# Optimization experiments

Measured on AMD Instinct MI355X. Metric: run time of the kernel, lower is better.

The kernel has to match this reference:

```python
import jax, jax.numpy as jnp
import numpy as np

N_NODES = 100000
N_EDGES = 1600000
HIDDEN = 128
N_CLASSES = 40
# torch.rand(1).item() in apply_randalign; fixed here for a deterministic reference
ALPHA = 0.62


def setup_inputs() -> dict:
    key = jax.random.key(0)
    ks = jax.random.split(key, 6)
    inputs = jax.random.normal(ks[0], (N_NODES, HIDDEN), jnp.float32)
    src = jax.random.randint(ks[1], (N_EDGES,), 0, N_NODES, jnp.int32)
    dst = jax.random.randint(ks[2], (N_EDGES,), 0, N_NODES, jnp.int32)
    s = 1.0 / np.sqrt(HIDDEN)
    W1 = jax.random.normal(ks[3], (HIDDEN, HIDDEN), jnp.float32) * s
    W2 = jax.random.normal(ks[4], (HIDDEN, HIDDEN), jnp.float32) * s
    W3 = jax.random.normal(ks[5], (HIDDEN, N_CLASSES), jnp.float32) * s
    return dict(inputs=inputs, src=src, dst=dst,
                W1=W1, b1=jnp.zeros((HIDDEN,), jnp.float32),
                W2=W2, b2=jnp.zeros((HIDDEN,), jnp.float32),
                W3=W3, b3=jnp.zeros((N_CLASSES,), jnp.float32))


def _graph_conv(x, W, b, src, dst):
    # DGL GraphConv, norm='both': D_dst^{-1/2} A D_src^{-1/2} X W + b
    n = x.shape[0]
    ones = jnp.ones(src.shape, x.dtype)
    deg_out = jnp.clip(jax.ops.segment_sum(ones, src, num_segments=n), 1.0)
    deg_in = jnp.clip(jax.ops.segment_sum(ones, dst, num_segments=n), 1.0)
    h = (x @ W) * (deg_out ** -0.5)[:, None]          # row scaling commutes with XW
    agg = jax.ops.segment_sum(h[src], dst, num_segments=n)
    return agg * (deg_in ** -0.5)[:, None] + b


def _randalign(h_prev, h_curr, alpha):
    norm_prev = jnp.linalg.norm(h_prev, axis=1, keepdims=True)
    norm_curr = jnp.linalg.norm(h_curr, axis=1, keepdims=True)
    scaled_prev = h_prev * (norm_curr / norm_prev)
    return alpha * h_curr + (1.0 - alpha) * scaled_prev


def reference(inputs, src, dst, W1, b1, W2, b2, W3, b3):
    # Faithful to source: layers[0] is never applied; loop runs over layers[1..-2].
    h = jax.nn.relu(_graph_conv(inputs, W1, b1, src, dst))      # i = 1
    h_next = jax.nn.relu(_graph_conv(h, W2, b2, src, dst))      # i = 2
    h = _randalign(h, h_next, ALPHA)
    logits = _graph_conv(h, W3, b3, src, dst)                   # final layer
    return logits
```

## Files before the change

kernel.cpp:

```cpp
#include <hip/hip_runtime.h>
#include <hip/hip_bf16.h>

#define HIDDEN 128
#define ALPHA_F 0.62f
#define CAP 64
#define BKT_BITS 9
#define BCAP 10240
#define CSTRIDE 136

typedef __attribute__((ext_vector_type(8))) short bf16x8;
typedef __attribute__((ext_vector_type(4))) float f32x4;

__device__ inline unsigned short f2bf(float f) {
  unsigned u = __float_as_uint(f);
  unsigned r = (u + 0x7fffu + ((u >> 16) & 1u)) >> 16;
  return (unsigned short)r;
}
__device__ inline float bf2f(unsigned short h) {
  return __uint_as_float((unsigned)h << 16);
}
__device__ inline float bflo(unsigned x) { return __uint_as_float(x << 16); }
__device__ inline float bfhi(unsigned x) { return __uint_as_float(x & 0xffff0000u); }

__device__ inline f32x4 mfma_bf16(bf16x8 a, bf16x8 b, f32x4 c) {
  return __builtin_amdgcn_mfma_f32_16x16x32_bf16(a, b, c, 0, 0, 0);
}

template <int CT>
__device__ void gemm_mfma_body(const float* __restrict__ A,
                               const unsigned short* __restrict__ WhT,
                               const unsigned short* __restrict__ WlT,
                               unsigned short* __restrict__ outp, int n, int NW, int gi,
                               unsigned* __restrict__ smem) {
  unsigned short* s16 = (unsigned short*)smem;
  const int t = threadIdx.x;
  const int wv = t >> 6, l = t & 63;
  const int lr = l & 15, lg = (l >> 4) & 3;
  const int rb = gi * 128;

  constexpr int WSLOTS = 4 * CT * 64;
  for (int s = t; s < WSLOTS; s += 256) {
    int sl = s & 63;
    int cc = s >> 6;
    int ct = cc % CT, c = cc / CT;
    int col = ct * 16 + (sl & 15);
    int k = c * 32 + ((sl >> 4) & 3) * 8;
    uint4 hv = *(const uint4*)&WhT[(size_t)col * HIDDEN + k];
    uint4 lv = *(const uint4*)&WlT[(size_t)col * HIDDEN + k];
    *(uint4*)&s16[(cc * 2 + 0) * 512 + sl * 8] = hv;
    *(uint4*)&s16[(cc * 2 + 1) * 512 + sl * 8] = lv;
  }

  f32x4 acc[2][CT];
#pragma unroll
  for (int rt = 0; rt < 2; rt++)
#pragma unroll
    for (int ct = 0; ct < CT; ct++)
#pragma unroll
      for (int e = 0; e < 4; e++) acc[rt][ct][e] = 0.f;

  __syncthreads();

  for (int c = 0; c < 4; c++) {
    bf16x8 ah[2], al[2];
#pragma unroll
    for (int rt = 0; rt < 2; rt++) {
      int rr = rb + wv * 32 + rt * 16 + lr;
      if (rr >= n) rr = n - 1;
      const float4* g = (const float4*)(A + (size_t)rr * HIDDEN + c * 32 + lg * 8);
      float4 v0 = g[0], v1 = g[1];
      float f[8] = {v0.x, v0.y, v0.z, v0.w, v1.x, v1.y, v1.z, v1.w};
#pragma unroll
      for (int q = 0; q < 8; q++) {
        unsigned short h = f2bf(f[q]);
        ah[rt][q] = (short)h;
        al[rt][q] = (short)f2bf(f[q] - bf2f(h));
      }
    }
#pragma unroll
    for (int ct = 0; ct < CT; ct++) {
      int cc = c * CT + ct;
      bf16x8 bh = *(const bf16x8*)&s16[(cc * 2 + 0) * 512 + l * 8];
      bf16x8 bl = *(const bf16x8*)&s16[(cc * 2 + 1) * 512 + l * 8];
#pragma unroll
      for (int rt = 0; rt < 2; rt++) {
        acc[rt][ct] = mfma_bf16(ah[rt], bh, acc[rt][ct]);
        acc[rt][ct] = mfma_bf16(al[rt], bh, acc[rt][ct]);
        acc[rt][ct] = mfma_bf16(ah[rt], bl, acc[rt][ct]);
      }
    }
  }

  __syncthreads();
  unsigned short* cr = s16 + wv * (32 * CSTRIDE);
#pragma unroll
  for (int rt = 0; rt < 2; rt++)
#pragma unroll
    for (int ct = 0; ct < CT; ct++)
#pragma unroll
      for (int r = 0; r < 4; r++)
        cr[(rt * 16 + lg * 4 + r) * CSTRIDE + ct * 16 + lr] = f2bf(acc[rt][ct][r]);
#pragma unroll
  for (int ps = 0; ps < 8; ps++) {
    int row_local = ps * 4 + lg;
    int orow = rb + wv * 32 + row_local;
    if (orow < n && lr * 8 < NW) {
      uint4 v = *(const uint4*)&cr[row_local * CSTRIDE + lr * 8];
      *(uint4*)&outp[(size_t)orow * NW + lr * 8] = v;
    }
  }
}

__global__ __launch_bounds__(256) void partition_kernel(
    const int* __restrict__ src, const int* __restrict__ dst, int E, int nbkt,
    unsigned* __restrict__ gcur1, unsigned* __restrict__ gcur2,
    unsigned* __restrict__ stg1, unsigned short* __restrict__ stg2, int pa_blocks,
    const float* __restrict__ W1, const float* __restrict__ W2, const float* __restrict__ W3,
    unsigned short* __restrict__ W1h, unsigned short* __restrict__ W1l,
    unsigned short* __restrict__ W2h, unsigned short* __restrict__ W2l,
    unsigned short* __restrict__ W3h, unsigned short* __restrict__ W3l, int NC) {
  const int t = threadIdx.x;
  const int bid = blockIdx.x;
  if (bid >= pa_blocks) {
    int r = bid - pa_blocks;
    const float* W = (r == 0) ? W1 : (r == 1) ? W2 : W3;
    unsigned short* Wh = (r == 0) ? W1h : (r == 1) ? W2h : W3h;
    unsigned short* Wl = (r == 0) ? W1l : (r == 1) ? W2l : W3l;
    int ncol = (r == 2) ? 64 : 128;
    int nw   = (r == 2) ? NC : 128;
    for (int idx = t; idx < ncol * HIDDEN; idx += 256) {
      int c = idx >> 7, k = idx & 127;
      float v = (c < nw) ? W[(size_t)k * nw + c] : 0.f;
      unsigned short hi = f2bf(v);
      Wh[idx] = hi;
      Wl[idx] = f2bf(v - bf2f(hi));
    }
    return;
  }
  __shared__ unsigned h1[256], h2[256], b1[256], b2[256];
  h1[t] = 0; h2[t] = 0;
  __syncthreads();
  const int chunk = (E + pa_blocks - 1) / pa_blocks;
  const int e0 = bid * chunk, e1 = min(e0 + chunk, E);
  for (int e = e0 + t; e < e1; e += 256) {
    atomicAdd(&h1[(unsigned)dst[e] >> BKT_BITS], 1u);
    atomicAdd(&h2[(unsigned)src[e] >> BKT_BITS], 1u);
  }
  __syncthreads();
  if (t < nbkt) {
    b1[t] = atomicAdd(&gcur1[t], h1[t]);
    b2[t] = atomicAdd(&gcur2[t], h2[t]);
  }
  h1[t] = 0; h2[t] = 0;
  __syncthreads();
  for (int e = e0 + t; e < e1; e += 256) {
    int s = src[e], d = dst[e];
    unsigned bk1 = (unsigned)d >> BKT_BITS;
    unsigned p1 = b1[bk1] + atomicAdd(&h1[bk1], 1u);
    if (p1 < BCAP) stg1[(size_t)bk1 * BCAP + p1] = ((unsigned)s << BKT_BITS) | ((unsigned)d & 511u);
    unsigned bk2 = (unsigned)s >> BKT_BITS;
    unsigned p2 = b2[bk2] + atomicAdd(&h2[bk2], 1u);
    if (p2 < BCAP) stg2[(size_t)bk2 * BCAP + p2] = (unsigned short)(s & 511);
  }
}

__global__ __launch_bounds__(256) void csr_and_gemm1_kernel(
    const unsigned* __restrict__ gcur1, const unsigned* __restrict__ gcur2,
    const unsigned* __restrict__ stg1, const unsigned short* __restrict__ stg2,
    int* __restrict__ csr, int* __restrict__ deg_in, int* __restrict__ deg_out,
    int n, int nbkt,
    const float* __restrict__ X,
    const unsigned short* __restrict__ W1h, const unsigned short* __restrict__ W1l,
    unsigned short* __restrict__ T1) {
  __shared__ __align__(16) unsigned smem[16384];
  const int bid = blockIdx.x;
  if (bid >= 2 * nbkt) {
    gemm_mfma_body<8>(X, W1h, W1l, T1, n, HIDDEN, bid - 2 * nbkt, smem);
    return;
  }
  int* cnt = (int*)smem;
  const int t = threadIdx.x;
  cnt[t] = 0; cnt[t + 256] = 0;
  __syncthreads();
  if (bid < nbkt) {
    const int b = bid;
    const int m = min((int)gcur1[b], BCAP);
    const int node0 = b << BKT_BITS;
    for (int i = t; i < m; i += 256) {
      unsigned val = stg1[(size_t)b * BCAP + i];
      int dl = val & 511;
      int s = (int)(val >> BKT_BITS);
      int pos = atomicAdd(&cnt[dl], 1);
      if (pos < CAP) csr[((size_t)(node0 + dl) << 6) + pos] = s;
    }
    __syncthreads();
    for (int u = t; u < 512; u += 256) {
      int node = node0 + u;
      if (node < n) deg_in[node] = cnt[u];
    }
  } else {
    const int b = bid - nbkt;
    const int m = min((int)gcur2[b], BCAP);
    const int node0 = b << BKT_BITS;
    for (int i = t; i < m; i += 256) {
      atomicAdd(&cnt[stg2[(size_t)b * BCAP + i]], 1);
    }
    __syncthreads();
    for (int u = t; u < 512; u += 256) {
      int node = node0 + u;
      if (node < n) deg_out[node] = cnt[u];
    }
  }
}

__global__ __launch_bounds__(256) void gemm2_kernel(
    const float* __restrict__ A,
    const unsigned short* __restrict__ Wh, const unsigned short* __restrict__ Wl,
    unsigned short* __restrict__ T, int n) {
  __shared__ __align__(16) unsigned smem[16384];
  gemm_mfma_body<8>(A, Wh, Wl, T, n, HIDDEN, blockIdx.x, smem);
}

__global__ __launch_bounds__(256) void gemm3_kernel(
    const float* __restrict__ A,
    const unsigned short* __restrict__ Wh, const unsigned short* __restrict__ Wl,
    unsigned short* __restrict__ T, int n) {
  __shared__ __align__(16) unsigned smem[9000];
  gemm_mfma_body<4>(A, Wh, Wl, T, n, 64, blockIdx.x, smem);
}

template <bool RA>
__global__ __launch_bounds__(256) void gather_conv_kernel(
    const unsigned* __restrict__ Tu, const int* __restrict__ csr,
    const int* __restrict__ deg_out, const int* __restrict__ deg_in,
    const float* __restrict__ bias, float* __restrict__ H, int n) {
  const int wv = threadIdx.x >> 6, l = threadIdx.x & 63;
  const int v = blockIdx.x * 4 + wv;
  if (v >= n) return;
  const int half = l >> 5, cg = l & 31;
  const int deg = deg_in[v];
  const int m = min(deg, CAP);
  int iu = (l < m) ? csr[((size_t)v << 6) + l] : 0;
  float wu = (l < m) ? rsqrtf((float)max(deg_out[iu], 1)) : 0.f;

  const uint2* Tr = (const uint2*)Tu;
  float a0 = 0.f, a1 = 0.f, a2 = 0.f, a3 = 0.f;
  float b0 = 0.f, b1 = 0.f, b2 = 0.f, b3 = 0.f;
  int j = 0;
  for (; j + 2 < m; j += 4) {
    int eA = j + half, eB = j + 2 + half;
    int uA = __shfl(iu, eA), uB = __shfl(iu, eB);
    float wA = __shfl(wu, eA), wB = __shfl(wu, eB);
    uint2 xA = Tr[(size_t)uA * 32 + cg];
    uint2 xB = Tr[(size_t)uB * 32 + cg];
    a0 = fmaf(wA, bflo(xA.x), a0); a1 = fmaf(wA, bfhi(xA.x), a1);
    a2 = fmaf(wA, bflo(xA.y), a2); a3 = fmaf(wA, bfhi(xA.y), a3);
    b0 = fmaf(wB, bflo(xB.x), b0); b1 = fmaf(wB, bfhi(xB.x), b1);
    b2 = fmaf(wB, bflo(xB.y), b2); b3 = fmaf(wB, bfhi(xB.y), b3);
  }
  for (; j < m; j += 2) {
    int eA = j + half;
    int uA = __shfl(iu, eA);
    float wA = __shfl(wu, eA);
    uint2 xA = Tr[(size_t)uA * 32 + cg];
    a0 = fmaf(wA, bflo(xA.x), a0); a1 = fmaf(wA, bfhi(xA.x), a1);
    a2 = fmaf(wA, bflo(xA.y), a2); a3 = fmaf(wA, bfhi(xA.y), a3);
  }
  a0 += b0; a1 += b1; a2 += b2; a3 += b3;
  a0 += __shfl_xor(a0, 32);
  a1 += __shfl_xor(a1, 32);
  a2 += __shfl_xor(a2, 32);
  a3 += __shfl_xor(a3, 32);

  float din = rsqrtf((float)max(deg, 1));
  float4 bias4 = ((const float4*)bias)[cg];
  float r0 = fmaxf(a0 * din + bias4.x, 0.f);
  float r1 = fmaxf(a1 * din + bias4.y, 0.f);
  float r2 = fmaxf(a2 * din + bias4.z, 0.f);
  float r3 = fmaxf(a3 * din + bias4.w, 0.f);

  if (RA) {
    float4 p = ((const float4*)(H + (size_t)v * HIDDEN))[cg];
    float sc = r0 * r0 + r1 * r1 + r2 * r2 + r3 * r3;
    float sp = p.x * p.x + p.y * p.y + p.z * p.z + p.w * p.w;
#pragma unroll
    for (int off = 1; off < 32; off <<= 1) {
      sc += __shfl_xor(sc, off);
      sp += __shfl_xor(sp, off);
    }
    float ratio = sqrtf(sc) / sqrtf(sp);
    r0 = ALPHA_F * r0 + (1.0f - ALPHA_F) * p.x * ratio;
    r1 = ALPHA_F * r1 + (1.0f - ALPHA_F) * p.y * ratio;
    r2 = ALPHA_F * r2 + (1.0f - ALPHA_F) * p.z * ratio;
    r3 = ALPHA_F * r3 + (1.0f - ALPHA_F) * p.w * ratio;
  }
  if (half == 0)
    ((float4*)(H + (size_t)v * HIDDEN))[cg] = make_float4(r0, r1, r2, r3);
}

__global__ __launch_bounds__(256) void gather_final_kernel(
    const unsigned* __restrict__ Tu3, const int* __restrict__ csr,
    const int* __restrict__ deg_out, const int* __restrict__ deg_in,
    const float* __restrict__ bias, float* __restrict__ out, int n, int NC) {
  const int wv = threadIdx.x >> 6, l = threadIdx.x & 63;
  const int v = blockIdx.x * 4 + wv;
  if (v >= n) return;
  const int q = l >> 4, cg = l & 15;
  const int deg = deg_in[v];
  const int m = min(deg, CAP);
  int iu = (l < m) ? csr[((size_t)v << 6) + l] : 0;
  float wu = (l < m) ? rsqrtf((float)max(deg_out[iu], 1)) : 0.f;

  const uint2* Tr = (const uint2*)Tu3;
  float a0 = 0.f, a1 = 0.f, a2 = 0.f, a3 = 0.f;
  for (int j = 0; j < m; j += 4) {
    int e = j + q;
    int u = __shfl(iu, e);
    float w = __shfl(wu, e);
    uint2 x = Tr[(size_t)u * 16 + cg];
    a0 = fmaf(w, bflo(x.x), a0); a1 = fmaf(w, bfhi(x.x), a1);
    a2 = fmaf(w, bflo(x.y), a2); a3 = fmaf(w, bfhi(x.y), a3);
  }
  a0 += __shfl_xor(a0, 16); a0 += __shfl_xor(a0, 32);
  a1 += __shfl_xor(a1, 16); a1 += __shfl_xor(a1, 32);
  a2 += __shfl_xor(a2, 16); a2 += __shfl_xor(a2, 32);
  a3 += __shfl_xor(a3, 16); a3 += __shfl_xor(a3, 32);
  if (l < 10) {
    float din = rsqrtf((float)max(deg, 1));
    float4 bias4 = ((const float4*)bias)[l];
    float4 o = make_float4(a0 * din + bias4.x, a1 * din + bias4.y,
                           a2 * din + bias4.z, a3 * din + bias4.w);
    *(float4*)(out + (size_t)v * NC + 4 * l) = o;
  }
}

extern "C" void kernel_launch(void* const* d_in, const int* in_sizes, int n_in,
                              void* d_out, int out_size, void* d_ws, size_t ws_size,
                              hipStream_t stream) {
  const float* X  = (const float*)d_in[0];
  const int* src  = (const int*)d_in[1];
  const int* dst  = (const int*)d_in[2];
  const float* W1 = (const float*)d_in[3];
  const float* b1 = (const float*)d_in[4];
  const float* W2 = (const float*)d_in[5];
  const float* b2 = (const float*)d_in[6];
  const float* W3 = (const float*)d_in[7];
  const float* b3 = (const float*)d_in[8];
  float* out = (float*)d_out;

  const int n = in_sizes[0] / HIDDEN;
  const int E = in_sizes[1];
  const int NC = in_sizes[8];
  const int nbkt = (n + 511) >> BKT_BITS;

  char* p = (char*)d_ws;
  auto alloc = [&](size_t bytes) {
    char* r = p;
    p += (bytes + 255) & ~(size_t)255;
    return r;
  };
  unsigned* gcur1 = (unsigned*)alloc(512 * 4);
  unsigned* gcur2 = gcur1 + 256;
  int* deg_out    = (int*)alloc((size_t)n * 4);
  int* deg_in     = (int*)alloc((size_t)n * 4);
  int* csr        = (int*)alloc((size_t)n * CAP * 4);
  unsigned short* stg2 = (unsigned short*)alloc((size_t)256 * BCAP * 2);
  unsigned* stg1  = (unsigned*)alloc((size_t)256 * BCAP * 4);
  unsigned short* BufT = (unsigned short*)alloc((size_t)n * HIDDEN * 2);
  float* BufB     = (float*)alloc((size_t)n * HIDDEN * 4);
  unsigned short* W1h = (unsigned short*)alloc(128 * 128 * 2);
  unsigned short* W1l = (unsigned short*)alloc(128 * 128 * 2);
  unsigned short* W2h = (unsigned short*)alloc(128 * 128 * 2);
  unsigned short* W2l = (unsigned short*)alloc(128 * 128 * 2);
  unsigned short* W3h = (unsigned short*)alloc(64 * 128 * 2);
  unsigned short* W3l = (unsigned short*)alloc(64 * 128 * 2);

  hipMemsetAsync(gcur1, 0, 512 * 4, stream);

  const int PA = 256;
  partition_kernel<<<PA + 3, 256, 0, stream>>>(src, dst, E, nbkt, gcur1, gcur2, stg1, stg2, PA,
                                               W1, W2, W3, W1h, W1l, W2h, W2l, W3h, W3l, NC);

  int gb = (n + 127) / 128;
  csr_and_gemm1_kernel<<<2 * nbkt + gb, 256, 0, stream>>>(gcur1, gcur2, stg1, stg2,
                                                          csr, deg_in, deg_out, n, nbkt,
                                                          X, W1h, W1l, BufT);
  int hb = (n + 3) / 4;
  gather_conv_kernel<false><<<hb, 256, 0, stream>>>(
      (const unsigned*)BufT, csr, deg_out, deg_in, b1, BufB, n);
  gemm2_kernel<<<gb, 256, 0, stream>>>(BufB, W2h, W2l, BufT, n);
  gather_conv_kernel<true><<<hb, 256, 0, stream>>>(
      (const unsigned*)BufT, csr, deg_out, deg_in, b2, BufB, n);
  gemm3_kernel<<<gb, 256, 0, stream>>>(BufB, W3h, W3l, BufT, n);
  gather_final_kernel<<<hb, 256, 0, stream>>>(
      (const unsigned*)BufT, csr, deg_out, deg_in, b3, out, n, NC);
}
```

Baseline: 316.1 us.

## Store hidden activations in bf16 and widen gather loads to 16 bytes

```diff
diff --git a/kernel.cpp b/kernel.cpp
--- a/kernel.cpp
+++ b/kernel.cpp
@@ -21,6 +21,9 @@
 }
 __device__ inline float bflo(unsigned x) { return __uint_as_float(x << 16); }
 __device__ inline float bfhi(unsigned x) { return __uint_as_float(x & 0xffff0000u); }
+__device__ inline unsigned bfpack(float a, float b) {
+  return (unsigned)f2bf(a) | ((unsigned)f2bf(b) << 16);
+}
 
 __device__ inline f32x4 mfma_bf16(bf16x8 a, bf16x8 b, f32x4 c) {
   return __builtin_amdgcn_mfma_f32_16x16x32_bf16(a, b, c, 0, 0, 0);
@@ -86,6 +89,82 @@
       for (int rt = 0; rt < 2; rt++) {
         acc[rt][ct] = mfma_bf16(ah[rt], bh, acc[rt][ct]);
         acc[rt][ct] = mfma_bf16(al[rt], bh, acc[rt][ct]);
+        acc[rt][ct] = mfma_bf16(ah[rt], bl, acc[rt][ct]);
+      }
+    }
+  }
+
+  __syncthreads();
+  unsigned short* cr = s16 + wv * (32 * CSTRIDE);
+#pragma unroll
+  for (int rt = 0; rt < 2; rt++)
+#pragma unroll
+    for (int ct = 0; ct < CT; ct++)
+#pragma unroll
+      for (int r = 0; r < 4; r++)
+        cr[(rt * 16 + lg * 4 + r) * CSTRIDE + ct * 16 + lr] = f2bf(acc[rt][ct][r]);
+#pragma unroll
+  for (int ps = 0; ps < 8; ps++) {
+    int row_local = ps * 4 + lg;
+    int orow = rb + wv * 32 + row_local;
+    if (orow < n && lr * 8 < NW) {
+      uint4 v = *(const uint4*)&cr[row_local * CSTRIDE + lr * 8];
+      *(uint4*)&outp[(size_t)orow * NW + lr * 8] = v;
+    }
+  }
+}
+
+template <int CT>
+__device__ void gemm_bf16A_body(const unsigned short* __restrict__ A,
+                                const unsigned short* __restrict__ WhT,
+                                const unsigned short* __restrict__ WlT,
+                                unsigned short* __restrict__ outp, int n, int NW, int gi,
+                                unsigned* __restrict__ smem) {
+  unsigned short* s16 = (unsigned short*)smem;
+  const int t = threadIdx.x;
+  const int wv = t >> 6, l = t & 63;
+  const int lr = l & 15, lg = (l >> 4) & 3;
+  const int rb = gi * 128;
+
+  constexpr int WSLOTS = 4 * CT * 64;
+  for (int s = t; s < WSLOTS; s += 256) {
+    int sl = s & 63;
+    int cc = s >> 6;
+    int ct = cc % CT, c = cc / CT;
+    int col = ct * 16 + (sl & 15);
+    int k = c * 32 + ((sl >> 4) & 3) * 8;
+    uint4 hv = *(const uint4*)&WhT[(size_t)col * HIDDEN + k];
+    uint4 lv = *(const uint4*)&WlT[(size_t)col * HIDDEN + k];
+    *(uint4*)&s16[(cc * 2 + 0) * 512 + sl * 8] = hv;
+    *(uint4*)&s16[(cc * 2 + 1) * 512 + sl * 8] = lv;
+  }
+
+  f32x4 acc[2][CT];
+#pragma unroll
+  for (int rt = 0; rt < 2; rt++)
+#pragma unroll
+    for (int ct = 0; ct < CT; ct++)
+#pragma unroll
+      for (int e = 0; e < 4; e++) acc[rt][ct][e] = 0.f;
+
+  __syncthreads();
+
+  for (int c = 0; c < 4; c++) {
+    bf16x8 ah[2];
+#pragma unroll
+    for (int rt = 0; rt < 2; rt++) {
+      int rr = rb + wv * 32 + rt * 16 + lr;
+      if (rr >= n) rr = n - 1;
+      ah[rt] = *(const bf16x8*)&A[(size_t)rr * HIDDEN + c * 32 + lg * 8];
+    }
+#pragma unroll
+    for (int ct = 0; ct < CT; ct++) {
+      int cc = c * CT + ct;
+      bf16x8 bh = *(const bf16x8*)&s16[(cc * 2 + 0) * 512 + l * 8];
+      bf16x8 bl = *(const bf16x8*)&s16[(cc * 2 + 1) * 512 + l * 8];
+#pragma unroll
+      for (int rt = 0; rt < 2; rt++) {
+        acc[rt][ct] = mfma_bf16(ah[rt], bh, acc[rt][ct]);
         acc[rt][ct] = mfma_bf16(ah[rt], bl, acc[rt][ct]);
       }
     }
@@ -214,94 +293,26 @@
 }
 
 __global__ __launch_bounds__(256) void gemm2_kernel(
-    const float* __restrict__ A,
+    const unsigned short* __restrict__ A,
     const unsigned short* __restrict__ Wh, const unsigned short* __restrict__ Wl,
     unsigned short* __restrict__ T, int n) {
   __shared__ __align__(16) unsigned smem[16384];
-  gemm_mfma_body<8>(A, Wh, Wl, T, n, HIDDEN, blockIdx.x, smem);
+  gemm_bf16A_body<8>(A, Wh, Wl, T, n, HIDDEN, blockIdx.x, smem);
 }
 
 __global__ __launch_bounds__(256) void gemm3_kernel(
-    const float* __restrict__ A,
+    const unsigned short* __restrict__ A,
     const unsigned short* __restrict__ Wh, const unsigned short* __restrict__ Wl,
     unsigned short* __restrict__ T, int n) {
   __shared__ __align__(16) unsigned smem[9000];
-  gemm_mfma_body<4>(A, Wh, Wl, T, n, 64, blockIdx.x, smem);
+  gemm_bf16A_body<4>(A, Wh, Wl, T, n, 64, blockIdx.x, smem);
 }
 
 template <bool RA>
 __global__ __launch_bounds__(256) void gather_conv_kernel(
-    const unsigned* __restrict__ Tu, const int* __restrict__ csr,
+    const uint4* __restrict__ Tr, const int* __restrict__ csr,
     const int* __restrict__ deg_out, const int* __restrict__ deg_in,
-    const float* __restrict__ bias, float* __restrict__ H, int n) {
-  const int wv = threadIdx.x >> 6, l = threadIdx.x & 63;
-  const int v = blockIdx.x * 4 + wv;
-  if (v >= n) return;
-  const int half = l >> 5, cg = l & 31;
-  const int deg = deg_in[v];
-  const int m = min(deg, CAP);
-  int iu = (l < m) ? csr[((size_t)v << 6) + l] : 0;
-  float wu = (l < m) ? rsqrtf((float)max(deg_out[iu], 1)) : 0.f;
-
-  const uint2* Tr = (const uint2*)Tu;
-  float a0 = 0.f, a1 = 0.f, a2 = 0.f, a3 = 0.f;
-  float b0 = 0.f, b1 = 0.f, b2 = 0.f, b3 = 0.f;
-  int j = 0;
-  for (; j + 2 < m; j += 4) {
-    int eA = j + half, eB = j + 2 + half;
-    int uA = __shfl(iu, eA), uB = __shfl(iu, eB);
-    float wA = __shfl(wu, eA), wB = __shfl(wu, eB);
-    uint2 xA = Tr[(size_t)uA * 32 + cg];
-    uint2 xB = Tr[(size_t)uB * 32 + cg];
-    a0 = fmaf(wA, bflo(xA.x), a0); a1 = fmaf(wA, bfhi(xA.x), a1);
-    a2 = fmaf(wA, bflo(xA.y), a2); a3 = fmaf(wA, bfhi(xA.y), a3);
-    b0 = fmaf(wB, bflo(xB.x), b0); b1 = fmaf(wB, bfhi(xB.x), b1);
-    b2 = fmaf(wB, bflo(xB.y), b2); b3 = fmaf(wB, bfhi(xB.y), b3);
-  }
-  for (; j < m; j += 2) {
-    int eA = j + half;
-    int uA = __shfl(iu, eA);
-    float wA = __shfl(wu, eA);
-    uint2 xA = Tr[(size_t)uA * 32 + cg];
-    a0 = fmaf(wA, bflo(xA.x), a0); a1 = fmaf(wA, bfhi(xA.x), a1);
-    a2 = fmaf(wA, bflo(xA.y), a2); a3 = fmaf(wA, bfhi(xA.y), a3);
-  }
-  a0 += b0; a1 += b1; a2 += b2; a3 += b3;
-  a0 += __shfl_xor(a0, 32);
-  a1 += __shfl_xor(a1, 32);
-  a2 += __shfl_xor(a2, 32);
-  a3 += __shfl_xor(a3, 32);
-
-  float din = rsqrtf((float)max(deg, 1));
-  float4 bias4 = ((const float4*)bias)[cg];
-  float r0 = fmaxf(a0 * din + bias4.x, 0.f);
-  float r1 = fmaxf(a1 * din + bias4.y, 0.f);
-  float r2 = fmaxf(a2 * din + bias4.z, 0.f);
-  float r3 = fmaxf(a3 * din + bias4.w, 0.f);
-
-  if (RA) {
-    float4 p = ((const float4*)(H + (size_t)v * HIDDEN))[cg];
-    float sc = r0 * r0 + r1 * r1 + r2 * r2 + r3 * r3;
-    float sp = p.x * p.x + p.y * p.y + p.z * p.z + p.w * p.w;
-#pragma unroll
-    for (int off = 1; off < 32; off <<= 1) {
-      sc += __shfl_xor(sc, off);
-      sp += __shfl_xor(sp, off);
-    }
-    float ratio = sqrtf(sc) / sqrtf(sp);
-    r0 = ALPHA_F * r0 + (1.0f - ALPHA_F) * p.x * ratio;
-    r1 = ALPHA_F * r1 + (1.0f - ALPHA_F) * p.y * ratio;
-    r2 = ALPHA_F * r2 + (1.0f - ALPHA_F) * p.z * ratio;
-    r3 = ALPHA_F * r3 + (1.0f - ALPHA_F) * p.w * ratio;
-  }
-  if (half == 0)
-    ((float4*)(H + (size_t)v * HIDDEN))[cg] = make_float4(r0, r1, r2, r3);
-}
-
-__global__ __launch_bounds__(256) void gather_final_kernel(
-    const unsigned* __restrict__ Tu3, const int* __restrict__ csr,
-    const int* __restrict__ deg_out, const int* __restrict__ deg_in,
-    const float* __restrict__ bias, float* __restrict__ out, int n, int NC) {
+    const float* __restrict__ bias, unsigned short* H, int n) {
   const int wv = threadIdx.x >> 6, l = threadIdx.x & 63;
   const int v = blockIdx.x * 4 + wv;
   if (v >= n) return;
@@ -311,26 +322,136 @@
   int iu = (l < m) ? csr[((size_t)v << 6) + l] : 0;
   float wu = (l < m) ? rsqrtf((float)max(deg_out[iu], 1)) : 0.f;
 
-  const uint2* Tr = (const uint2*)Tu3;
-  float a0 = 0.f, a1 = 0.f, a2 = 0.f, a3 = 0.f;
-  for (int j = 0; j < m; j += 4) {
+  float a0 = 0.f, a1 = 0.f, a2 = 0.f, a3 = 0.f, a4 = 0.f, a5 = 0.f, a6 = 0.f, a7 = 0.f;
+  float b0 = 0.f, b1 = 0.f, b2 = 0.f, b3 = 0.f, b4 = 0.f, b5 = 0.f, b6 = 0.f, b7 = 0.f;
+  int j = 0;
+  for (; j + 8 <= m; j += 8) {
+    int eA = j + q, eB = j + 4 + q;
+    int uA = __shfl(iu, eA), uB = __shfl(iu, eB);
+    float wA = __shfl(wu, eA), wB = __shfl(wu, eB);
+    uint4 xA = Tr[(size_t)uA * 16 + cg];
+    uint4 xB = Tr[(size_t)uB * 16 + cg];
+    a0 = fmaf(wA, bflo(xA.x), a0); a1 = fmaf(wA, bfhi(xA.x), a1);
+    a2 = fmaf(wA, bflo(xA.y), a2); a3 = fmaf(wA, bfhi(xA.y), a3);
+    a4 = fmaf(wA, bflo(xA.z), a4); a5 = fmaf(wA, bfhi(xA.z), a5);
+    a6 = fmaf(wA, bflo(xA.w), a6); a7 = fmaf(wA, bfhi(xA.w), a7);
+    b0 = fmaf(wB, bflo(xB.x), b0); b1 = fmaf(wB, bfhi(xB.x), b1);
+    b2 = fmaf(wB, bflo(xB.y), b2); b3 = fmaf(wB, bfhi(xB.y), b3);
+    b4 = fmaf(wB, bflo(xB.z), b4); b5 = fmaf(wB, bfhi(xB.z), b5);
+    b6 = fmaf(wB, bflo(xB.w), b6); b7 = fmaf(wB, bfhi(xB.w), b7);
+  }
+  for (; j < m; j += 4) {
     int e = j + q;
     int u = __shfl(iu, e);
     float w = __shfl(wu, e);
-    uint2 x = Tr[(size_t)u * 16 + cg];
+    uint4 x = Tr[(size_t)u * 16 + cg];
     a0 = fmaf(w, bflo(x.x), a0); a1 = fmaf(w, bfhi(x.x), a1);
     a2 = fmaf(w, bflo(x.y), a2); a3 = fmaf(w, bfhi(x.y), a3);
-  }
-  a0 += __shfl_xor(a0, 16); a0 += __shfl_xor(a0, 32);
-  a1 += __shfl_xor(a1, 16); a1 += __shfl_xor(a1, 32);
-  a2 += __shfl_xor(a2, 16); a2 += __shfl_xor(a2, 32);
-  a3 += __shfl_xor(a3, 16); a3 += __shfl_xor(a3, 32);
-  if (l < 10) {
+    a4 = fmaf(w, bflo(x.z), a4); a5 = fmaf(w, bfhi(x.z), a5);
+    a6 = fmaf(w, bflo(x.w), a6); a7 = fmaf(w, bfhi(x.w), a7);
+  }
+  a0 += b0; a1 += b1; a2 += b2; a3 += b3; a4 += b4; a5 += b5; a6 += b6; a7 += b7;
+#pragma unroll
+  for (int off = 16; off < 64; off <<= 1) {
+    a0 += __shfl_xor(a0, off); a1 += __shfl_xor(a1, off);
+    a2 += __shfl_xor(a2, off); a3 += __shfl_xor(a3, off);
+    a4 += __shfl_xor(a4, off); a5 += __shfl_xor(a5, off);
+    a6 += __shfl_xor(a6, off); a7 += __shfl_xor(a7, off);
+  }
+
+  float din = rsqrtf((float)max(deg, 1));
+  float4 bA = ((const float4*)bias)[cg * 2];
+  float4 bB = ((const float4*)bias)[cg * 2 + 1];
+  float r0 = fmaxf(a0 * din + bA.x, 0.f);
+  float r1 = fmaxf(a1 * din + bA.y, 0.f);
+  float r2 = fmaxf(a2 * din + bA.z, 0.f);
+  float r3 = fmaxf(a3 * din + bA.w, 0.f);
+  float r4 = fmaxf(a4 * din + bB.x, 0.f);
+  float r5 = fmaxf(a5 * din + bB.y, 0.f);
+  float r6 = fmaxf(a6 * din + bB.z, 0.f);
+  float r7 = fmaxf(a7 * din + bB.w, 0.f);
+
+  if (RA) {
+    uint4 hp = ((const uint4*)(H + (size_t)v * HIDDEN))[cg];
+    float p0 = bflo(hp.x), p1 = bfhi(hp.x), p2 = bflo(hp.y), p3 = bfhi(hp.y);
+    float p4 = bflo(hp.z), p5 = bfhi(hp.z), p6 = bflo(hp.w), p7 = bfhi(hp.w);
+    float sc = r0*r0 + r1*r1 + r2*r2 + r3*r3 + r4*r4 + r5*r5 + r6*r6 + r7*r7;
+    float sp = p0*p0 + p1*p1 + p2*p2 + p3*p3 + p4*p4 + p5*p5 + p6*p6 + p7*p7;
+#pragma unroll
+    for (int off = 1; off < 16; off <<= 1) {
+      sc += __shfl_xor(sc, off);
+      sp += __shfl_xor(sp, off);
+    }
+    float ratio = sqrtf(sc) / sqrtf(sp);
+    const float am = 1.0f - ALPHA_F;
+    r0 = ALPHA_F * r0 + am * p0 * ratio; r1 = ALPHA_F * r1 + am * p1 * ratio;
+    r2 = ALPHA_F * r2 + am * p2 * ratio; r3 = ALPHA_F * r3 + am * p3 * ratio;
+    r4 = ALPHA_F * r4 + am * p4 * ratio; r5 = ALPHA_F * r5 + am * p5 * ratio;
+    r6 = ALPHA_F * r6 + am * p6 * ratio; r7 = ALPHA_F * r7 + am * p7 * ratio;
+  }
+  if (q == 0) {
+    uint4 pk = make_uint4(bfpack(r0, r1), bfpack(r2, r3), bfpack(r4, r5), bfpack(r6, r7));
+    ((uint4*)(H + (size_t)v * HIDDEN))[cg] = pk;
+  }
+}
+
+__global__ __launch_bounds__(256) void gather_final_kernel(
+    const uint4* __restrict__ Tr3, const int* __restrict__ csr,
+    const int* __restrict__ deg_out, const int* __restrict__ deg_in,
+    const float* __restrict__ bias, float* __restrict__ out, int n, int NC) {
+  const int wv = threadIdx.x >> 6, l = threadIdx.x & 63;
+  const int v = blockIdx.x * 4 + wv;
+  if (v >= n) return;
+  const int o = l >> 3, cg = l & 7;
+  const int deg = deg_in[v];
+  const int m = min(deg, CAP);
+  int iu = (l < m) ? csr[((size_t)v << 6) + l] : 0;
+  float wu = (l < m) ? rsqrtf((float)max(deg_out[iu], 1)) : 0.f;
+
+  float a0 = 0.f, a1 = 0.f, a2 = 0.f, a3 = 0.f, a4 = 0.f, a5 = 0.f, a6 = 0.f, a7 = 0.f;
+  float b0 = 0.f, b1 = 0.f, b2 = 0.f, b3 = 0.f, b4 = 0.f, b5 = 0.f, b6 = 0.f, b7 = 0.f;
+  int j = 0;
+  for (; j + 16 <= m; j += 16) {
+    int eA = j + o, eB = j + 8 + o;
+    int uA = __shfl(iu, eA), uB = __shfl(iu, eB);
+    float wA = __shfl(wu, eA), wB = __shfl(wu, eB);
+    uint4 xA = Tr3[(size_t)uA * 8 + cg];
+    uint4 xB = Tr3[(size_t)uB * 8 + cg];
+    a0 = fmaf(wA, bflo(xA.x), a0); a1 = fmaf(wA, bfhi(xA.x), a1);
+    a2 = fmaf(wA, bflo(xA.y), a2); a3 = fmaf(wA, bfhi(xA.y), a3);
+    a4 = fmaf(wA, bflo(xA.z), a4); a5 = fmaf(wA, bfhi(xA.z), a5);
+    a6 = fmaf(wA, bflo(xA.w), a6); a7 = fmaf(wA, bfhi(xA.w), a7);
+    b0 = fmaf(wB, bflo(xB.x), b0); b1 = fmaf(wB, bfhi(xB.x), b1);
+    b2 = fmaf(wB, bflo(xB.y), b2); b3 = fmaf(wB, bfhi(xB.y), b3);
+    b4 = fmaf(wB, bflo(xB.z), b4); b5 = fmaf(wB, bfhi(xB.z), b5);
+    b6 = fmaf(wB, bflo(xB.w), b6); b7 = fmaf(wB, bfhi(xB.w), b7);
+  }
+  for (; j < m; j += 8) {
+    int e = j + o;
+    int u = __shfl(iu, e);
+    float w = __shfl(wu, e);
+    uint4 x = Tr3[(size_t)u * 8 + cg];
+    a0 = fmaf(w, bflo(x.x), a0); a1 = fmaf(w, bfhi(x.x), a1);
+    a2 = fmaf(w, bflo(x.y), a2); a3 = fmaf(w, bfhi(x.y), a3);
+    a4 = fmaf(w, bflo(x.z), a4); a5 = fmaf(w, bfhi(x.z), a5);
+    a6 = fmaf(w, bflo(x.w), a6); a7 = fmaf(w, bfhi(x.w), a7);
+  }
+  a0 += b0; a1 += b1; a2 += b2; a3 += b3; a4 += b4; a5 += b5; a6 += b6; a7 += b7;
+#pragma unroll
+  for (int off = 8; off < 64; off <<= 1) {
+    a0 += __shfl_xor(a0, off); a1 += __shfl_xor(a1, off);
+    a2 += __shfl_xor(a2, off); a3 += __shfl_xor(a3, off);
+    a4 += __shfl_xor(a4, off); a5 += __shfl_xor(a5, off);
+    a6 += __shfl_xor(a6, off); a7 += __shfl_xor(a7, off);
+  }
+  if (l < 5) {
     float din = rsqrtf((float)max(deg, 1));
-    float4 bias4 = ((const float4*)bias)[l];
-    float4 o = make_float4(a0 * din + bias4.x, a1 * din + bias4.y,
-                           a2 * din + bias4.z, a3 * din + bias4.w);
-    *(float4*)(out + (size_t)v * NC + 4 * l) = o;
+    float4 bA = ((const float4*)bias)[l * 2];
+    float4 bB = ((const float4*)bias)[l * 2 + 1];
+    float4 oA = make_float4(a0 * din + bA.x, a1 * din + bA.y, a2 * din + bA.z, a3 * din + bA.w);
+    float4 oB = make_float4(a4 * din + bB.x, a5 * din + bB.y, a6 * din + bB.z, a7 * din + bB.w);
+    *(float4*)(out + (size_t)v * NC + 8 * l) = oA;
+    *(float4*)(out + (size_t)v * NC + 8 * l + 4) = oB;
   }
 }
 
@@ -367,7 +488,7 @@
   unsigned short* stg2 = (unsigned short*)alloc((size_t)256 * BCAP * 2);
   unsigned* stg1  = (unsigned*)alloc((size_t)256 * BCAP * 4);
   unsigned short* BufT = (unsigned short*)alloc((size_t)n * HIDDEN * 2);
-  float* BufB     = (float*)alloc((size_t)n * HIDDEN * 4);
+  unsigned short* BufH = (unsigned short*)alloc((size_t)n * HIDDEN * 2);
   unsigned short* W1h = (unsigned short*)alloc(128 * 128 * 2);
   unsigned short* W1l = (unsigned short*)alloc(128 * 128 * 2);
   unsigned short* W2h = (unsigned short*)alloc(128 * 128 * 2);
@@ -387,11 +508,11 @@
                                                           X, W1h, W1l, BufT);
   int hb = (n + 3) / 4;
   gather_conv_kernel<false><<<hb, 256, 0, stream>>>(
-      (const unsigned*)BufT, csr, deg_out, deg_in, b1, BufB, n);
-  gemm2_kernel<<<gb, 256, 0, stream>>>(BufB, W2h, W2l, BufT, n);
+      (const uint4*)BufT, csr, deg_out, deg_in, b1, BufH, n);
+  gemm2_kernel<<<gb, 256, 0, stream>>>(BufH, W2h, W2l, BufT, n);
   gather_conv_kernel<true><<<hb, 256, 0, stream>>>(
-      (const unsigned*)BufT, csr, deg_out, deg_in, b2, BufB, n);
-  gemm3_kernel<<<gb, 256, 0, stream>>>(BufB, W3h, W3l, BufT, n);
+      (const uint4*)BufT, csr, deg_out, deg_in, b2, BufH, n);
+  gemm3_kernel<<<gb, 256, 0, stream>>>(BufH, W3h, W3l, BufT, n);
   gather_final_kernel<<<hb, 256, 0, stream>>>(
-      (const unsigned*)BufT, csr, deg_out, deg_in, b3, out, n, NC);
-}
+      (const uint4*)BufT, csr, deg_out, deg_in, b3, out, n, NC);
+}
```

Result: faster. 277.5 us (-12.2%).
